# Kernel optimization log

Measured on AMD Instinct MI355X. Metric: run time of the kernel, lower is better.

## Reference

```python
import jax, jax.numpy as jnp
import numpy as np

QUERY_DIM = 1024
CONTEXT_DIM = 1024
HEADS = 8
DIM_HEAD = 64
INNER = HEADS * DIM_HEAD  # 512
B, NQ, NC = 2, 1024, 1024


def setup_inputs() -> dict:
    key = jax.random.key(0)
    ks = jax.random.split(key, 9)
    s_in_q = 1.0 / np.sqrt(QUERY_DIM)
    s_in_c = 1.0 / np.sqrt(CONTEXT_DIM)
    s_in_o = 1.0 / np.sqrt(INNER)
    return {
        "x": jax.random.normal(ks[0], (B, NQ, QUERY_DIM), dtype=jnp.float32),
        "context": jax.random.normal(ks[1], (B, NC, CONTEXT_DIM), dtype=jnp.float32),
        "mask": jnp.ones((B, NQ + NC), dtype=bool),
        # weights stored as [in, out] (transpose of torch Linear.weight)
        "Wq": jax.random.normal(ks[2], (QUERY_DIM, INNER), dtype=jnp.float32) * s_in_q,
        "Wk": jax.random.normal(ks[3], (CONTEXT_DIM, INNER), dtype=jnp.float32) * s_in_c,
        "Wv": jax.random.normal(ks[4], (CONTEXT_DIM, INNER), dtype=jnp.float32) * s_in_c,
        "Wv_self": jax.random.normal(ks[5], (QUERY_DIM, INNER), dtype=jnp.float32) * s_in_q,
        "Wo": jax.random.normal(ks[6], (INNER, QUERY_DIM), dtype=jnp.float32) * s_in_o,
        "bo": jnp.zeros((QUERY_DIM,), dtype=jnp.float32),
    }


def reference(x, context, mask, Wq, Wk, Wv, Wv_self, Wo, bo):
    h, d = HEADS, DIM_HEAD
    scale = d ** (-0.5)
    b, nq, _ = x.shape

    q = x @ Wq                                   # [b, nq, inner]
    k = context @ Wk                             # [b, nc, inner]
    v_cross = context @ Wv                       # [b, nc, inner]
    v_self = jax.lax.stop_gradient(x @ Wv_self)  # detached in original

    qc = jnp.concatenate([q, k], axis=1)         # [b, n, inner], n = nq+nc
    kc = qc                                      # k = q.clone()
    v = jnp.concatenate([v_self, v_cross], axis=1)

    def split_heads(t):
        bb, n, _ = t.shape
        return t.reshape(bb, n, h, d).transpose(0, 2, 1, 3)  # [b, h, n, d]

    qh, kh, vh = split_heads(qc), split_heads(kc), split_heads(v)

    sim = jnp.einsum('bhid,bhjd->bhij', qh, kh) * scale      # [b, h, n, n]
    neg = -jnp.finfo(sim.dtype).max
    sim = jnp.where(mask[:, None, None, :], sim, neg)
    attn = jax.nn.softmax(sim, axis=-1)
    out = jnp.einsum('bhij,bhjd->bhid', attn, vh)            # [b, h, n, d]

    gated = out[:, :, :nq, :]                                # first nq queries
    gated = gated.transpose(0, 2, 1, 3).reshape(b, nq, h * d)
    return gated @ Wo + bo
```

## Files before the change

kernel.cpp:

```cpp
#include <hip/hip_runtime.h>

typedef __bf16 bf16;
typedef __bf16 bf16x8 __attribute__((ext_vector_type(8)));
typedef __bf16 bf16x4v __attribute__((ext_vector_type(4)));
typedef float f32x4 __attribute__((ext_vector_type(4)));
typedef short short4v __attribute__((ext_vector_type(4)));

__device__ __forceinline__ f32x4 mfma16(bf16x8 a, bf16x8 b, f32x4 c) {
  return __builtin_amdgcn_mfma_f32_16x16x32_bf16(a, b, c, 0, 0, 0);
}

__device__ __forceinline__ f32x4 mfma16k16(bf16x4v a, bf16x4v b, f32x4 c) {
#if __has_builtin(__builtin_amdgcn_mfma_f32_16x16x16_bf16)
  return __builtin_amdgcn_mfma_f32_16x16x16_bf16(a, b, c, 0, 0, 0);
#else
  return __builtin_amdgcn_mfma_f32_16x16x16bf16_1k(
      __builtin_bit_cast(short4v, a), __builtin_bit_cast(short4v, b), c, 0, 0, 0);
#endif
}

__device__ __forceinline__ void load16_lds(const void* g, void* l) {
  __builtin_amdgcn_global_load_lds(
      (const __attribute__((address_space(1))) void*)(unsigned long long)g,
      (__attribute__((address_space(3))) void*)(unsigned long long)l, 16, 0, 0);
}

__global__ __launch_bounds__(256) void prep(
    const float4* __restrict__ x, const float4* __restrict__ c,
    bf16x4v* __restrict__ xb, bf16x4v* __restrict__ cb,
    const float* __restrict__ Wq, const float* __restrict__ Wk,
    const float* __restrict__ Wv, const float* __restrict__ Wvs,
    const float* __restrict__ Wo,
    bf16* __restrict__ WqT, bf16* __restrict__ WkT, bf16* __restrict__ WvT,
    bf16* __restrict__ WsT, bf16* __restrict__ WoT) {
  int bid = blockIdx.x;
  if (bid < 4096) {
    int i = bid * 256 + threadIdx.x;
    const float4* s; bf16x4v* d; int j;
    if (i < 524288) { s = x; d = xb; j = i; }
    else            { s = c; d = cb; j = i - 524288; }
    float4 f = s[j];
    bf16x4v o;
    o[0] = (bf16)f.x; o[1] = (bf16)f.y; o[2] = (bf16)f.z; o[3] = (bf16)f.w;
    d[j] = o;
    return;
  }
  __shared__ float tile[32][33];
  int bid2 = bid - 4096;
  int z = bid2 >> 10, rem = bid2 & 1023;
  const float* src; bf16* dst; int K, N;
  switch (z) {
    case 0: src = Wq;  dst = WqT; K = 1024; N = 512;  break;
    case 1: src = Wk;  dst = WkT; K = 1024; N = 512;  break;
    case 2: src = Wv;  dst = WvT; K = 1024; N = 512;  break;
    case 3: src = Wvs; dst = WsT; K = 1024; N = 512;  break;
    default: src = Wo; dst = WoT; K = 512;  N = 1024; break;
  }
  int n0 = (rem & 31) * 32, k0 = (rem >> 5) * 32;
  if (n0 >= N || k0 >= K) return;
  int tx = threadIdx.x & 31, ty = threadIdx.x >> 5;
#pragma unroll
  for (int i = 0; i < 32; i += 8)
    tile[ty + i][tx] = src[(size_t)(k0 + ty + i) * N + n0 + tx];
  __syncthreads();
#pragma unroll
  for (int i = 0; i < 32; i += 8)
    dst[(size_t)(n0 + ty + i) * K + k0 + tx] = (bf16)tile[tx][ty + i];
}

__global__ __launch_bounds__(256) void qkv_gemm(
    const bf16* __restrict__ xb, const bf16* __restrict__ cb,
    const bf16* __restrict__ WqT, const bf16* __restrict__ WkT,
    const bf16* __restrict__ WvT, const bf16* __restrict__ WsT,
    bf16* __restrict__ qc, bf16* __restrict__ vT) {
  __shared__ __align__(16) bf16 As[128 * 32];
  __shared__ __align__(16) bf16 Bs[64 * 32];
  int m0 = blockIdx.y * 128, n0 = blockIdx.x * 64;
  int b = m0 >> 11, r0 = m0 & 2047;
  bool rowHalf = r0 < 1024;
  const bf16* Abase = rowHalf ? (xb + (size_t)(b * 1024 + r0) * 1024)
                              : (cb + (size_t)(b * 1024 + (r0 - 1024)) * 1024);
  bool colHalf = n0 < 512;
  const bf16* WT = colHalf ? (rowHalf ? WqT : WkT) : (rowHalf ? WsT : WvT);
  int nW = colHalf ? n0 : n0 - 512;
  const bf16* Bbase = WT + (size_t)nW * 1024;

  int tid = threadIdx.x;
  int lane = tid & 63, w = tid >> 6;
  int low = lane & 15, quad = lane >> 4;
  f32x4 acc[4][2] = {};

  for (int kk = 0; kk < 1024; kk += 32) {
#pragma unroll
    for (int t = 0; t < 2; t++) {
      int c = t * 256 + tid;
      int row = c >> 2, k8 = (c & 3) * 8;
      load16_lds(Abase + (size_t)row * 1024 + kk + k8, As + t * 2048 + w * 512);
    }
    {
      int row = tid >> 2, k8 = (tid & 3) * 8;
      load16_lds(Bbase + (size_t)row * 1024 + kk + k8, Bs + w * 512);
    }
    __syncthreads();
    bf16x8 af[4], bfr[2];
    int mb = (w >> 1) * 64 + low;
#pragma unroll
    for (int mi = 0; mi < 4; mi++) af[mi] = *(const bf16x8*)&As[(mb + mi * 16) * 32 + quad * 8];
#pragma unroll
    for (int ni = 0; ni < 2; ni++)
      bfr[ni] = *(const bf16x8*)&Bs[((w & 1) * 32 + ni * 16 + low) * 32 + quad * 8];
#pragma unroll
    for (int mi = 0; mi < 4; mi++)
#pragma unroll
      for (int ni = 0; ni < 2; ni++) acc[mi][ni] = mfma16(af[mi], bfr[ni], acc[mi][ni]);
    __syncthreads();
  }

#pragma unroll
  for (int mi = 0; mi < 4; mi++) {
    int rowg = m0 + (w >> 1) * 64 + mi * 16 + quad * 4;
#pragma unroll
    for (int ni = 0; ni < 2; ni++) {
      int col = n0 + (w & 1) * 32 + ni * 16 + low;
      if (col < 512) {
#pragma unroll
        for (int r = 0; r < 4; r++)
          qc[(size_t)(rowg + r) * 512 + col] = (bf16)acc[mi][ni][r];
      } else {
        int d = col - 512;
        int bb = rowg >> 11, key = rowg & 2047;
        bf16x4v pk;
#pragma unroll
        for (int r = 0; r < 4; r++) pk[r] = (bf16)acc[mi][ni][r];
        *(bf16x4v*)&vT[((size_t)(bb * 512 + d)) * 2048 + key] = pk;
      }
    }
  }
}

__global__ __launch_bounds__(256) void attn_part(const bf16* __restrict__ qc,
                                                 const bf16* __restrict__ vT,
                                                 float* __restrict__ Opart,
                                                 float* __restrict__ lpart) {
  __shared__ __align__(16) bf16 Ks[64 * 64];
  __shared__ __align__(16) bf16 Vs[64 * 64];
  int bh = blockIdx.y, b = bh >> 3, h = bh & 7;
  int q0 = blockIdx.x * 64;
  int ch = blockIdx.z;
  int tid = threadIdx.x, lane = tid & 63, w = tid >> 6;
  int low = lane & 15, quad = lane >> 4;
  const float SC = 0.125f * 1.44269504f;

  const bf16* Qrow = qc + ((size_t)(b * 2048) + q0 + w * 16 + low) * 512 + h * 64;
  bf16x8 qf0 = *(const bf16x8*)(Qrow + quad * 8);
  bf16x8 qf1 = *(const bf16x8*)(Qrow + 32 + quad * 8);

  f32x4 accT[4] = {};
  float l_lane = 0.f;

  const bf16* Kg = qc + (size_t)(b * 2048) * 512 + h * 64;
  const bf16* Vg = vT + (size_t)(b * 512 + h * 64) * 2048;

  for (int k0 = ch * 512; k0 < ch * 512 + 512; k0 += 64) {
    __syncthreads();
#pragma unroll
    for (int t = 0; t < 2; t++) {
      int p = t * 256 + tid;
      int r = p >> 3, c8 = (p & 7) ^ (r & 7);
      load16_lds(Kg + (size_t)(k0 + r) * 512 + c8 * 8, Ks + (t * 256 + w * 64) * 8);
      load16_lds(Vg + (size_t)r * 2048 + k0 + c8 * 8, Vs + (t * 256 + w * 64) * 8);
    }
    __syncthreads();

    bf16x4v pk[4];
#pragma unroll
    for (int kt = 0; kt < 4; kt++) {
      int row = kt * 16 + low, sw = row & 7;
      bf16x8 ka0 = *(const bf16x8*)&Ks[row * 64 + (quad ^ sw) * 8];
      bf16x8 ka1 = *(const bf16x8*)&Ks[row * 64 + ((4 + quad) ^ sw) * 8];
      f32x4 s = {0.f, 0.f, 0.f, 0.f};
      s = mfma16(ka0, qf0, s);
      s = mfma16(ka1, qf1, s);
      float p0 = exp2f(s[0] * SC), p1 = exp2f(s[1] * SC);
      float p2 = exp2f(s[2] * SC), p3 = exp2f(s[3] * SC);
      l_lane += (p0 + p1) + (p2 + p3);
      bf16x4v v;
      v[0] = (bf16)p0; v[1] = (bf16)p1; v[2] = (bf16)p2; v[3] = (bf16)p3;
      pk[kt] = v;
    }

#pragma unroll
    for (int dt = 0; dt < 4; dt++) {
      int row = dt * 16 + low, sw = row & 7;
#pragma unroll
      for (int kt = 0; kt < 4; kt++) {
        int c8 = kt * 2 + (quad >> 1);
        bf16x4v va =
            *(const bf16x4v*)&Vs[row * 64 + ((c8 ^ sw)) * 8 + (quad & 1) * 4];
        accT[dt] = mfma16k16(va, pk[kt], accT[dt]);
      }
    }
  }

  l_lane += __shfl_xor(l_lane, 16, 64);
  l_lane += __shfl_xor(l_lane, 32, 64);
  int q = q0 + w * 16 + low;
  if (quad == 0) lpart[((size_t)bh * 1024 + q) * 4 + ch] = l_lane;

  float* Od = Opart + (((size_t)bh * 1024 + q) * 4 + ch) * 64;
#pragma unroll
  for (int dt = 0; dt < 4; dt++)
    *(f32x4*)(Od + dt * 16 + quad * 4) = accT[dt];
}

__global__ __launch_bounds__(256) void attn_comb(const float* __restrict__ Opart,
                                                 const float* __restrict__ lpart,
                                                 bf16* __restrict__ gated) {
  int bh = blockIdx.y, b = bh >> 3, h = bh & 7;
  int q = blockIdx.x * 64 + (threadIdx.x >> 2);
  int dbase = (threadIdx.x & 3) * 16;
  const float* lp = lpart + ((size_t)bh * 1024 + q) * 4;
  float inv = 1.f / (lp[0] + lp[1] + lp[2] + lp[3]);
  const f32x4* Op = (const f32x4*)(Opart + ((size_t)bh * 1024 + q) * 256);
  bf16* og = gated + ((size_t)(b * 1024) + q) * 512 + h * 64 + dbase;
#pragma unroll
  for (int j = 0; j < 4; j++) {
    int di = dbase / 4 + j;
    f32x4 a0 = Op[di], a1 = Op[16 + di], a2 = Op[32 + di], a3 = Op[48 + di];
    bf16x4v o;
#pragma unroll
    for (int e = 0; e < 4; e++)
      o[e] = (bf16)((a0[e] + a1[e] + a2[e] + a3[e]) * inv);
    *(bf16x4v*)(og + j * 4) = o;
  }
}

__global__ __launch_bounds__(256) void out_gemm(const bf16* __restrict__ gated,
                                                const bf16* __restrict__ WoT,
                                                const float* __restrict__ bo,
                                                float* __restrict__ out) {
  __shared__ __align__(16) bf16 As[64 * 32];
  __shared__ __align__(16) bf16 Bs[64 * 32];
  int m0 = blockIdx.y * 64, n0 = blockIdx.x * 64;
  int tid = threadIdx.x, lane = tid & 63, w = tid >> 6;
  int low = lane & 15, quad = lane >> 4;
  const bf16* Ab = gated + (size_t)m0 * 512;
  const bf16* Bb = WoT + (size_t)n0 * 512;
  f32x4 acc[2][2] = {};

  for (int kk = 0; kk < 512; kk += 32) {
    int row = tid >> 2, k8 = (tid & 3) * 8;
    load16_lds(Ab + (size_t)row * 512 + kk + k8, As + w * 512);
    load16_lds(Bb + (size_t)row * 512 + kk + k8, Bs + w * 512);
    __syncthreads();
    bf16x8 af[2], bfr[2];
#pragma unroll
    for (int mi = 0; mi < 2; mi++)
      af[mi] = *(const bf16x8*)&As[((w >> 1) * 32 + mi * 16 + low) * 32 + quad * 8];
#pragma unroll
    for (int ni = 0; ni < 2; ni++)
      bfr[ni] = *(const bf16x8*)&Bs[((w & 1) * 32 + ni * 16 + low) * 32 + quad * 8];
#pragma unroll
    for (int mi = 0; mi < 2; mi++)
#pragma unroll
      for (int ni = 0; ni < 2; ni++) acc[mi][ni] = mfma16(af[mi], bfr[ni], acc[mi][ni]);
    __syncthreads();
  }

#pragma unroll
  for (int mi = 0; mi < 2; mi++) {
    int rowg = m0 + (w >> 1) * 32 + mi * 16 + quad * 4;
#pragma unroll
    for (int ni = 0; ni < 2; ni++) {
      int col = n0 + (w & 1) * 32 + ni * 16 + low;
      float bias = bo[col];
#pragma unroll
      for (int r = 0; r < 4; r++)
        out[(size_t)(rowg + r) * 1024 + col] = acc[mi][ni][r] + bias;
    }
  }
}

extern "C" void kernel_launch(void* const* d_in, const int* in_sizes, int n_in,
                              void* d_out, int out_size, void* d_ws, size_t ws_size,
                              hipStream_t stream) {
  const float* x   = (const float*)d_in[0];
  const float* ctx = (const float*)d_in[1];
  const float* Wq  = (const float*)d_in[3];
  const float* Wk  = (const float*)d_in[4];
  const float* Wv  = (const float*)d_in[5];
  const float* Wvs = (const float*)d_in[6];
  const float* Wo  = (const float*)d_in[7];
  const float* bo  = (const float*)d_in[8];
  float* out = (float*)d_out;

  bf16* xb  = (bf16*)d_ws;
  bf16* cb  = xb + 2097152;
  bf16* WqT = cb + 2097152;
  bf16* WkT = WqT + 524288;
  bf16* WvT = WkT + 524288;
  bf16* WsT = WvT + 524288;
  bf16* WoT = WsT + 524288;
  bf16* qcb = WoT + 524288;
  bf16* vTb = qcb + 2097152;
  bf16* gb  = vTb + 2097152;
  float* Opart = (float*)(gb + 1048576);
  float* lb    = Opart + 4194304;

  prep<<<9216, 256, 0, stream>>>((const float4*)x, (const float4*)ctx,
                                 (bf16x4v*)xb, (bf16x4v*)cb,
                                 Wq, Wk, Wv, Wvs, Wo, WqT, WkT, WvT, WsT, WoT);
  qkv_gemm<<<dim3(16, 32), 256, 0, stream>>>(xb, cb, WqT, WkT, WvT, WsT, qcb, vTb);
  attn_part<<<dim3(16, 16, 4), 256, 0, stream>>>(qcb, vTb, Opart, lb);
  attn_comb<<<dim3(16, 16), 256, 0, stream>>>(Opart, lb, gb);
  out_gemm<<<dim3(16, 32), 256, 0, stream>>>(gb, WoT, bo, out);
}
```

Measured before the change: 141.4 us.

## Widen GEMM K-tile with swizzled LDS, double attention query tile, vectorize transpose stores

Three separate changes. The QKV GEMM now loads a 64-wide K slice per iteration into XOR-swizzled shared memory, which halves the number of barriers and avoids bank conflicts. The attention partial kernel now handles 128 queries per block, two 16-row groups per wave, so each K/V tile loaded into LDS is reused twice; this halves the grid to 512 blocks and raises register pressure. The weight-transpose prep now writes bf16x4 vectors instead of scalar stores.

```diff
diff --git a/kernel.cpp b/kernel.cpp
--- a/kernel.cpp
+++ b/kernel.cpp
@@ -63,9 +63,11 @@
   for (int i = 0; i < 32; i += 8)
     tile[ty + i][tx] = src[(size_t)(k0 + ty + i) * N + n0 + tx];
   __syncthreads();
-#pragma unroll
-  for (int i = 0; i < 32; i += 8)
-    dst[(size_t)(n0 + ty + i) * K + k0 + tx] = (bf16)tile[tx][ty + i];
+  int n = threadIdx.x >> 3, k4 = (threadIdx.x & 7) * 4;
+  bf16x4v o4;
+#pragma unroll
+  for (int e = 0; e < 4; e++) o4[e] = (bf16)tile[k4 + e][n];
+  *(bf16x4v*)&dst[(size_t)(n0 + n) * K + k0 + k4] = o4;
 }
 
 __global__ __launch_bounds__(256) void qkv_gemm(
@@ -73,8 +75,8 @@
     const bf16* __restrict__ WqT, const bf16* __restrict__ WkT,
     const bf16* __restrict__ WvT, const bf16* __restrict__ WsT,
     bf16* __restrict__ qc, bf16* __restrict__ vT) {
-  __shared__ __align__(16) bf16 As[128 * 32];
-  __shared__ __align__(16) bf16 Bs[64 * 32];
+  __shared__ __align__(16) bf16 As[128 * 64];
+  __shared__ __align__(16) bf16 Bs[64 * 64];
   int m0 = blockIdx.y * 128, n0 = blockIdx.x * 64;
   int b = m0 >> 11, r0 = m0 & 2047;
   bool rowHalf = r0 < 1024;
@@ -90,29 +92,39 @@
   int low = lane & 15, quad = lane >> 4;
   f32x4 acc[4][2] = {};
 
-  for (int kk = 0; kk < 1024; kk += 32) {
+  for (int kk = 0; kk < 1024; kk += 64) {
+#pragma unroll
+    for (int t = 0; t < 4; t++) {
+      int p = t * 256 + tid;
+      int row = p >> 3, c8 = (p & 7) ^ (row & 7);
+      load16_lds(Abase + (size_t)row * 1024 + kk + c8 * 8, As + (t * 256 + w * 64) * 8);
+    }
 #pragma unroll
     for (int t = 0; t < 2; t++) {
-      int c = t * 256 + tid;
-      int row = c >> 2, k8 = (c & 3) * 8;
-      load16_lds(Abase + (size_t)row * 1024 + kk + k8, As + t * 2048 + w * 512);
-    }
-    {
-      int row = tid >> 2, k8 = (tid & 3) * 8;
-      load16_lds(Bbase + (size_t)row * 1024 + kk + k8, Bs + w * 512);
-    }
-    __syncthreads();
-    bf16x8 af[4], bfr[2];
-    int mb = (w >> 1) * 64 + low;
-#pragma unroll
-    for (int mi = 0; mi < 4; mi++) af[mi] = *(const bf16x8*)&As[(mb + mi * 16) * 32 + quad * 8];
-#pragma unroll
-    for (int ni = 0; ni < 2; ni++)
-      bfr[ni] = *(const bf16x8*)&Bs[((w & 1) * 32 + ni * 16 + low) * 32 + quad * 8];
-#pragma unroll
-    for (int mi = 0; mi < 4; mi++)
-#pragma unroll
-      for (int ni = 0; ni < 2; ni++) acc[mi][ni] = mfma16(af[mi], bfr[ni], acc[mi][ni]);
+      int p = t * 256 + tid;
+      int row = p >> 3, c8 = (p & 7) ^ (row & 7);
+      load16_lds(Bbase + (size_t)row * 1024 + kk + c8 * 8, Bs + (t * 256 + w * 64) * 8);
+    }
+    __syncthreads();
+#pragma unroll
+    for (int kk2 = 0; kk2 < 2; kk2++) {
+      bf16x8 af[4], bfr[2];
+      int mb = (w >> 1) * 64 + low;
+#pragma unroll
+      for (int mi = 0; mi < 4; mi++) {
+        int row = mb + mi * 16;
+        af[mi] = *(const bf16x8*)&As[row * 64 + ((kk2 * 4 + quad) ^ (row & 7)) * 8];
+      }
+#pragma unroll
+      for (int ni = 0; ni < 2; ni++) {
+        int row = (w & 1) * 32 + ni * 16 + low;
+        bfr[ni] = *(const bf16x8*)&Bs[row * 64 + ((kk2 * 4 + quad) ^ (row & 7)) * 8];
+      }
+#pragma unroll
+      for (int mi = 0; mi < 4; mi++)
+#pragma unroll
+        for (int ni = 0; ni < 2; ni++) acc[mi][ni] = mfma16(af[mi], bfr[ni], acc[mi][ni]);
+    }
     __syncthreads();
   }
 
@@ -145,18 +157,22 @@
   __shared__ __align__(16) bf16 Ks[64 * 64];
   __shared__ __align__(16) bf16 Vs[64 * 64];
   int bh = blockIdx.y, b = bh >> 3, h = bh & 7;
-  int q0 = blockIdx.x * 64;
+  int q0 = blockIdx.x * 128;
   int ch = blockIdx.z;
   int tid = threadIdx.x, lane = tid & 63, w = tid >> 6;
   int low = lane & 15, quad = lane >> 4;
   const float SC = 0.125f * 1.44269504f;
 
-  const bf16* Qrow = qc + ((size_t)(b * 2048) + q0 + w * 16 + low) * 512 + h * 64;
-  bf16x8 qf0 = *(const bf16x8*)(Qrow + quad * 8);
-  bf16x8 qf1 = *(const bf16x8*)(Qrow + 32 + quad * 8);
-
-  f32x4 accT[4] = {};
-  float l_lane = 0.f;
+  const bf16* Qrow = qc + ((size_t)(b * 2048) + q0 + w * 32 + low) * 512 + h * 64;
+  bf16x8 qf[2][2];
+#pragma unroll
+  for (int g = 0; g < 2; g++) {
+    qf[g][0] = *(const bf16x8*)(Qrow + (size_t)g * 16 * 512 + quad * 8);
+    qf[g][1] = *(const bf16x8*)(Qrow + (size_t)g * 16 * 512 + 32 + quad * 8);
+  }
+
+  f32x4 accT[2][4] = {};
+  float l_lane[2] = {0.f, 0.f};
 
   const bf16* Kg = qc + (size_t)(b * 2048) * 512 + h * 64;
   const bf16* Vg = vT + (size_t)(b * 512 + h * 64) * 2048;
@@ -172,21 +188,24 @@
     }
     __syncthreads();
 
-    bf16x4v pk[4];
+    bf16x4v pk[2][4];
 #pragma unroll
     for (int kt = 0; kt < 4; kt++) {
       int row = kt * 16 + low, sw = row & 7;
       bf16x8 ka0 = *(const bf16x8*)&Ks[row * 64 + (quad ^ sw) * 8];
       bf16x8 ka1 = *(const bf16x8*)&Ks[row * 64 + ((4 + quad) ^ sw) * 8];
-      f32x4 s = {0.f, 0.f, 0.f, 0.f};
-      s = mfma16(ka0, qf0, s);
-      s = mfma16(ka1, qf1, s);
-      float p0 = exp2f(s[0] * SC), p1 = exp2f(s[1] * SC);
-      float p2 = exp2f(s[2] * SC), p3 = exp2f(s[3] * SC);
-      l_lane += (p0 + p1) + (p2 + p3);
-      bf16x4v v;
-      v[0] = (bf16)p0; v[1] = (bf16)p1; v[2] = (bf16)p2; v[3] = (bf16)p3;
-      pk[kt] = v;
+#pragma unroll
+      for (int g = 0; g < 2; g++) {
+        f32x4 s = {0.f, 0.f, 0.f, 0.f};
+        s = mfma16(ka0, qf[g][0], s);
+        s = mfma16(ka1, qf[g][1], s);
+        float p0 = exp2f(s[0] * SC), p1 = exp2f(s[1] * SC);
+        float p2 = exp2f(s[2] * SC), p3 = exp2f(s[3] * SC);
+        l_lane[g] += (p0 + p1) + (p2 + p3);
+        bf16x4v v;
+        v[0] = (bf16)p0; v[1] = (bf16)p1; v[2] = (bf16)p2; v[3] = (bf16)p3;
+        pk[g][kt] = v;
+      }
     }
 
 #pragma unroll
@@ -197,20 +216,24 @@
         int c8 = kt * 2 + (quad >> 1);
         bf16x4v va =
             *(const bf16x4v*)&Vs[row * 64 + ((c8 ^ sw)) * 8 + (quad & 1) * 4];
-        accT[dt] = mfma16k16(va, pk[kt], accT[dt]);
-      }
-    }
-  }
-
-  l_lane += __shfl_xor(l_lane, 16, 64);
-  l_lane += __shfl_xor(l_lane, 32, 64);
-  int q = q0 + w * 16 + low;
-  if (quad == 0) lpart[((size_t)bh * 1024 + q) * 4 + ch] = l_lane;
-
-  float* Od = Opart + (((size_t)bh * 1024 + q) * 4 + ch) * 64;
-#pragma unroll
-  for (int dt = 0; dt < 4; dt++)
-    *(f32x4*)(Od + dt * 16 + quad * 4) = accT[dt];
+#pragma unroll
+        for (int g = 0; g < 2; g++)
+          accT[g][dt] = mfma16k16(va, pk[g][kt], accT[g][dt]);
+      }
+    }
+  }
+
+#pragma unroll
+  for (int g = 0; g < 2; g++) {
+    l_lane[g] += __shfl_xor(l_lane[g], 16, 64);
+    l_lane[g] += __shfl_xor(l_lane[g], 32, 64);
+    int q = q0 + w * 32 + g * 16 + low;
+    if (quad == 0) lpart[((size_t)bh * 1024 + q) * 4 + ch] = l_lane[g];
+    float* Od = Opart + (((size_t)bh * 1024 + q) * 4 + ch) * 64;
+#pragma unroll
+    for (int dt = 0; dt < 4; dt++)
+      *(f32x4*)(Od + dt * 16 + quad * 4) = accT[g][dt];
+  }
 }
 
 __global__ __launch_bounds__(256) void attn_comb(const float* __restrict__ Opart,
@@ -311,7 +334,7 @@
                                  (bf16x4v*)xb, (bf16x4v*)cb,
                                  Wq, Wk, Wv, Wvs, Wo, WqT, WkT, WvT, WsT, WoT);
   qkv_gemm<<<dim3(16, 32), 256, 0, stream>>>(xb, cb, WqT, WkT, WvT, WsT, qcb, vTb);
-  attn_part<<<dim3(16, 16, 4), 256, 0, stream>>>(qcb, vTb, Opart, lb);
+  attn_part<<<dim3(8, 16, 4), 256, 0, stream>>>(qcb, vTb, Opart, lb);
   attn_comb<<<dim3(16, 16), 256, 0, stream>>>(Opart, lb, gb);
   out_gemm<<<dim3(16, 32), 256, 0, stream>>>(gb, WoT, bo, out);
 }
```

Measured after the change: 137.8 us. -2.5%, faster.
